# Kernel tuning notes

Hardware: AMD Instinct MI355X
Metric: run time of the kernel (lower is better)

Reference implementation:

```python
import jax, jax.numpy as jnp
import numpy as np

NUM_HEADS = 16
HEAD_DIM = 64  # hidden_size 1024 / 16 heads


def setup_inputs() -> dict:
    key = jax.random.key(0)
    ks = jax.random.split(key, 4)
    B, S, H = 2, 2048, 1024
    scale = 0.02
    return {
        "hidden_states": jax.random.normal(ks[0], (B, S, H), jnp.float32),
        "attention_mask": jnp.zeros((B, 1, 1, S), jnp.float32),  # additive mask
        "Wq": jax.random.normal(ks[1], (H, H), jnp.float32) * scale,
        "bq": jnp.zeros((H,), jnp.float32),
        "Wk": jax.random.normal(ks[2], (H, H), jnp.float32) * scale,
        "bk": jnp.zeros((H,), jnp.float32),
        "Wv": jax.random.normal(ks[3], (H, H), jnp.float32) * scale,
        "bv": jnp.zeros((H,), jnp.float32),
    }


def _split_heads(x):
    B, S, H = x.shape
    return x.reshape(B, S, NUM_HEADS, HEAD_DIM).transpose(0, 2, 1, 3)  # [B,h,S,dh]


def reference(hidden_states, attention_mask, Wq, bq, Wk, bk, Wv, bv):
    q = _split_heads(hidden_states @ Wq + bq)
    k = _split_heads(hidden_states @ Wk + bk)
    v = _split_heads(hidden_states @ Wv + bv)
    # scaled dot-product scores [B,h,S,S]
    scores = jnp.einsum("bhqd,bhkd->bhqk", q, k) / np.sqrt(HEAD_DIM).astype(np.float32)
    scores = scores + attention_mask  # additive mask, broadcast [B,1,1,S]
    probs = jax.nn.softmax(scores, axis=-1)  # dropout prob = 0.0
    ctx = jnp.einsum("bhqk,bhkd->bhqd", probs, v)
    B, h, S, dh = ctx.shape
    return ctx.transpose(0, 2, 1, 3).reshape(B, S, h * dh)  # [B,S,hidden]
```

## Files before the change

kernel.cpp:

```cpp
#include <hip/hip_runtime.h>
#include <hip/hip_bf16.h>


typedef __bf16 bf16x8 __attribute__((ext_vector_type(8)));
typedef __bf16 bf16x4 __attribute__((ext_vector_type(4)));
typedef float f32x4 __attribute__((ext_vector_type(4)));
typedef float f32x16 __attribute__((ext_vector_type(16)));
typedef int i32x4 __attribute__((ext_vector_type(4)));

static constexpr int H = 1024;
static constexpr int S = 2048;
static constexpr int NH = 16;
static constexpr int DH = 64;
static constexpr float L2E = 1.4426950408889634f;

#if __has_builtin(__builtin_amdgcn_exp2f)
#define EXP2F(x) __builtin_amdgcn_exp2f(x)
#else
#define EXP2F(x) __builtin_exp2f(x)
#endif

__device__ inline void gll16(const void* g, void* l) {
  __builtin_amdgcn_global_load_lds(
      (const __attribute__((address_space(1))) void*)g,
      (__attribute__((address_space(3))) void*)l, 16, 0, 0);
}

__device__ inline int pack2bf(float lo, float hi) {
  unsigned short a = __builtin_bit_cast(unsigned short, (__bf16)lo);
  unsigned short b = __builtin_bit_cast(unsigned short, (__bf16)hi);
  return (int)(((unsigned)b << 16) | (unsigned)a);
}

__device__ inline void plswap(int& a, int& b) {
  asm volatile("v_permlane32_swap_b32 %0, %1" : "+v"(a), "+v"(b));
}

__global__ __launch_bounds__(256) void convert_kernel(
    const float* __restrict__ X, const float* __restrict__ W0,
    const float* __restrict__ W1, const float* __restrict__ W2,
    __bf16* __restrict__ Xb, __bf16* __restrict__ Wt) {
  __shared__ float T[64][65];
  const int bid = blockIdx.x, tid = threadIdx.x;
  if (bid < 2048) {
    size_t i = ((size_t)bid * 256 + tid) * 8;
    float4 f0 = *(const float4*)(X + i);
    float4 f1 = *(const float4*)(X + i + 4);
    bf16x8 o;
    o[0] = (__bf16)f0.x; o[1] = (__bf16)f0.y; o[2] = (__bf16)f0.z; o[3] = (__bf16)f0.w;
    o[4] = (__bf16)f1.x; o[5] = (__bf16)f1.y; o[6] = (__bf16)f1.z; o[7] = (__bf16)f1.w;
    *(bf16x8*)(Xb + i) = o;
    return;
  }
  const int wid = bid - 2048;
  const int z = wid >> 8, t = wid & 255;
  const int k0 = (t >> 4) * 64, n0 = (t & 15) * 64;
  const float* W = z == 0 ? W0 : (z == 1 ? W1 : W2);
  __bf16* Wo = Wt + (size_t)z * H * H;
#pragma unroll
  for (int it = 0; it < 4; ++it) {
    int r = it * 16 + (tid >> 4), c = (tid & 15) * 4;
    *(float4*)&T[r][c] = *(const float4*)&W[(size_t)(k0 + r) * H + n0 + c];
  }
  __syncthreads();
#pragma unroll
  for (int it = 0; it < 4; ++it) {
    int n = it * 16 + (tid >> 4), c0 = (tid & 15) * 4;
    bf16x4 o;
#pragma unroll
    for (int j = 0; j < 4; ++j) o[j] = (__bf16)T[c0 + j][n];
    *(bf16x4*)&Wo[(size_t)(n0 + n) * H + k0 + c0] = o;
  }
}

__global__ __launch_bounds__(256, 3) void qkv_gemm_kernel(
    const __bf16* __restrict__ Xb, const __bf16* __restrict__ Wt,
    const float* __restrict__ bq, const float* __restrict__ bk,
    const float* __restrict__ bv,
    __bf16* __restrict__ Qt, __bf16* __restrict__ K, __bf16* __restrict__ Vt)
{
  __shared__ __bf16 As[128 * 64];
  __shared__ __bf16 Bs[128 * 64];

  const int tid = threadIdx.x, lane = tid & 63, w = tid >> 6;
  const int quad = lane >> 4, l16 = lane & 15;

  const int lin = blockIdx.x + 24 * blockIdx.y;
  const int swz = (lin & 7) * 96 + (lin >> 3);
  const int bx = swz >> 5;
  const int by = swz & 31;
  const int wsel = bx >> 3;
  const int n0 = (bx & 7) * 128;
  const int m0 = by * 128;
  const int wr = w & 1, wc = w >> 1;

  const __bf16* Wsel = Wt + (size_t)wsel * H * H;
  const float* bias = wsel == 0 ? bq : (wsel == 1 ? bk : bv);

  const __bf16* aptr[4];
  const __bf16* bptr[4];
#pragma unroll
  for (int i = 0; i < 4; ++i) {
    int s = w * 256 + i * 64 + lane;
    int row = s >> 3, col = s & 7, sc = col ^ (row & 7);
    aptr[i] = Xb + (size_t)(m0 + row) * H + sc * 8;
    bptr[i] = Wsel + (size_t)(n0 + row) * H + sc * 8;
  }

  f32x4 acc[4][4] = {};

  for (int k0 = 0; k0 < H; k0 += 64) {
    __syncthreads();
#pragma unroll
    for (int i = 0; i < 4; ++i) {
      gll16(aptr[i] + k0, &As[(w * 256 + i * 64) * 8]);
      gll16(bptr[i] + k0, &Bs[(w * 256 + i * 64) * 8]);
    }
    __syncthreads();
#pragma unroll
    for (int kc = 0; kc < 2; ++kc) {
      bf16x8 af[4], bfr[4];
#pragma unroll
      for (int t = 0; t < 4; ++t) {
        int ra = wr * 64 + t * 16 + l16;
        af[t] = *(const bf16x8*)&As[ra * 64 + (((kc * 4 + quad) ^ (ra & 7)) * 8)];
        int rb = wc * 64 + t * 16 + l16;
        bfr[t] = *(const bf16x8*)&Bs[rb * 64 + (((kc * 4 + quad) ^ (rb & 7)) * 8)];
      }
#pragma unroll
      for (int t = 0; t < 4; ++t)
#pragma unroll
        for (int u = 0; u < 4; ++u)
          acc[t][u] = __builtin_amdgcn_mfma_f32_16x16x32_bf16(af[t], bfr[u], acc[t][u], 0, 0, 0);
    }
  }

  const float qscale = 0.125f * L2E;
#pragma unroll
  for (int u = 0; u < 4; ++u) {
    int n = n0 + wc * 64 + u * 16 + l16;
    int head = n >> 6, d = n & 63;
    float bias_v = bias[n];
#pragma unroll
    for (int t = 0; t < 4; ++t) {
      int srow = m0 + wr * 64 + t * 16 + quad * 4;
      int b = srow >> 11, si = srow & (S - 1);
      int bh = b * NH + head;
      if (wsel == 1) {
        __bf16* dst = K + ((size_t)bh * S + si) * DH + d;
#pragma unroll
        for (int r = 0; r < 4; ++r)
          dst[(size_t)r * DH] = (__bf16)(acc[t][u][r] + bias_v);
      } else {
        float scl = wsel == 0 ? qscale : 1.0f;
        __bf16* outp = wsel == 0 ? Qt : Vt;
        bf16x4 o;
#pragma unroll
        for (int r = 0; r < 4; ++r) o[r] = (__bf16)((acc[t][u][r] + bias_v) * scl);
        *(bf16x4*)&outp[((size_t)bh * DH + d) * S + si] = o;
      }
    }
  }
}

__global__ __launch_bounds__(256, 4) void attn_kernel(
    const __bf16* __restrict__ Qt, const __bf16* __restrict__ K,
    const __bf16* __restrict__ Vt, const float* __restrict__ mask,
    float* __restrict__ out)
{
  __shared__ __bf16 SM[20480];
  __bf16* Ksb = SM;
  __bf16* Vsb = SM + 8192;
  float*  Ms  = (float*)(SM + 16384);

  const int tid = threadIdx.x, lane = tid & 63, w = tid >> 6;
  const int l31 = lane & 31, hi = lane >> 5;
  const int wl = w & 1, wh = w >> 1;

  const int lin = blockIdx.y * 32 + blockIdx.x;
  const int v = (lin & 7) * 128 + (lin >> 3);
  const int bh = v >> 5, b = bh >> 4, h = bh & 15;
  const int q0 = (v & 31) * 64;

  const __bf16* Qb = Qt + (size_t)bh * DH * S;
  const __bf16* Kb = K + (size_t)bh * S * DH;
  const __bf16* Vb = Vt + (size_t)bh * DH * S;
  const float* mb = mask + (size_t)b * S;

  {
    int idx = tid * 8;
    float4 m0v = *(const float4*)&mb[idx];
    float4 m1v = *(const float4*)&mb[idx + 4];
    float4 s0v = {m0v.x * L2E, m0v.y * L2E, m0v.z * L2E, m0v.w * L2E};
    float4 s1v = {m1v.x * L2E, m1v.y * L2E, m1v.z * L2E, m1v.w * L2E};
    *(float4*)&Ms[idx] = s0v;
    *(float4*)&Ms[idx + 4] = s1v;
  }

  const int q = q0 + wl * 32 + l31;
  bf16x8 qf[4];
#pragma unroll
  for (int kc = 0; kc < 4; ++kc)
#pragma unroll
    for (int j = 0; j < 8; ++j)
      qf[kc][j] = Qb[(size_t)(kc * 16 + hi * 8 + j) * S + q];

  const int kvbase = wh * 1024;
  const __bf16* kptr[4];
  const __bf16* vptr[4];
#pragma unroll
  for (int i = 0; i < 4; ++i) {
    int s = wl * 256 + i * 64 + lane;
    int row = s >> 3, col = s & 7, sc = col ^ (row & 7);
    kptr[i] = Kb + (size_t)(kvbase + row) * DH + sc * 8;
    vptr[i] = Vb + (size_t)row * S + kvbase + sc * 8;
  }

  f32x16 o0 = {}, o1 = {};
  float dl = 0.0f;

  for (int st = 0; st < 16; ++st) {
    __syncthreads();
#pragma unroll
    for (int i = 0; i < 4; ++i) {
      gll16(kptr[i] + (size_t)st * 64 * DH,
            &Ksb[wh * 4096 + (wl * 256 + i * 64 + lane) * 8]);
      gll16(vptr[i] + st * 64,
            &Vsb[wh * 4096 + (wl * 256 + i * 64 + lane) * 8]);
    }
    __syncthreads();
    const __bf16* Kc = &Ksb[wh * 4096];
    const __bf16* Vc = &Vsb[wh * 4096];
    const int kvabs = kvbase + st * 64;

#pragma unroll
    for (int kvsub = 0; kvsub < 2; ++kvsub) {
      const int rk = kvsub * 32 + l31;
      f32x16 cc;
#pragma unroll
      for (int g = 0; g < 4; ++g) {
        float4 m4 = *(const float4*)&Ms[kvabs + kvsub * 32 + g * 8 + hi * 4];
        cc[4 * g + 0] = m4.x; cc[4 * g + 1] = m4.y;
        cc[4 * g + 2] = m4.z; cc[4 * g + 3] = m4.w;
      }
      __builtin_amdgcn_s_setprio(1);
#pragma unroll
      for (int kc = 0; kc < 4; ++kc) {
        bf16x8 af = *(const bf16x8*)&Kc[rk * 64 + (((kc * 2 + hi) ^ (l31 & 7)) * 8)];
        cc = __builtin_amdgcn_mfma_f32_32x32x16_bf16(af, qf[kc], cc, 0, 0, 0);
      }
      __builtin_amdgcn_s_setprio(0);

      float p[16];
#pragma unroll
      for (int r = 0; r < 16; ++r) { p[r] = EXP2F(cc[r]); dl += p[r]; }
      int a0 = pack2bf(p[0],  p[1]),  b0 = pack2bf(p[2],  p[3]);
      int a1 = pack2bf(p[4],  p[5]),  b1 = pack2bf(p[6],  p[7]);
      int a2 = pack2bf(p[8],  p[9]),  b2 = pack2bf(p[10], p[11]);
      int a3 = pack2bf(p[12], p[13]), b3 = pack2bf(p[14], p[15]);
      plswap(a0, a1); plswap(b0, b1);
      plswap(a2, a3); plswap(b2, b3);
      i32x4 pi0 = {a0, b0, a1, b1};
      i32x4 pi1 = {a2, b2, a3, b3};
      bf16x8 pf0 = __builtin_bit_cast(bf16x8, pi0);
      bf16x8 pf1 = __builtin_bit_cast(bf16x8, pi1);

      __builtin_amdgcn_s_setprio(1);
#pragma unroll
      for (int pp = 0; pp < 2; ++pp) {
        const int pc = kvsub * 2 + pp;
        const bf16x8 pf = pp ? pf1 : pf0;
        bf16x8 vf0 = *(const bf16x8*)&Vc[l31 * 64 + (((pc * 2 + hi) ^ (l31 & 7)) * 8)];
        o0 = __builtin_amdgcn_mfma_f32_32x32x16_bf16(vf0, pf, o0, 0, 0, 0);
        bf16x8 vf1 = *(const bf16x8*)&Vc[(32 + l31) * 64 + (((pc * 2 + hi) ^ (l31 & 7)) * 8)];
        o1 = __builtin_amdgcn_mfma_f32_32x32x16_bf16(vf1, pf, o1, 0, 0, 0);
      }
      __builtin_amdgcn_s_setprio(0);
    }
  }

  float lsum = dl + __shfl_xor(dl, 32);

  __syncthreads();
  float* Os = (float*)SM;
  float* Ls = (float*)(SM + 16384);
  const int qi = wl * 32 + l31;
  if (wh == 1) {
#pragma unroll
    for (int g = 0; g < 4; ++g) {
      int s0 = (2 * g + hi) ^ (l31 & 7);
      float4 t0 = {o0[4 * g + 0], o0[4 * g + 1], o0[4 * g + 2], o0[4 * g + 3]};
      *(float4*)&Os[qi * 64 + s0 * 4] = t0;
      int s1 = (8 + 2 * g + hi) ^ (l31 & 7);
      float4 t1 = {o1[4 * g + 0], o1[4 * g + 1], o1[4 * g + 2], o1[4 * g + 3]};
      *(float4*)&Os[qi * 64 + s1 * 4] = t1;
    }
    if (hi == 0) Ls[qi] = lsum;
  }
  __syncthreads();
  if (wh == 0) {
    float ltot = lsum + Ls[qi];
    float invl = 1.0f / ltot;
#pragma unroll
    for (int g = 0; g < 4; ++g) {
      int d0 = g * 8 + hi * 4;
      int s0 = (2 * g + hi) ^ (l31 & 7);
      float4 u0 = *(const float4*)&Os[qi * 64 + s0 * 4];
      float4 r0 = {(o0[4 * g + 0] + u0.x) * invl, (o0[4 * g + 1] + u0.y) * invl,
                   (o0[4 * g + 2] + u0.z) * invl, (o0[4 * g + 3] + u0.w) * invl};
      *(float4*)&out[((size_t)b * S + q) * H + h * DH + d0] = r0;
      int s1 = (8 + 2 * g + hi) ^ (l31 & 7);
      float4 u1 = *(const float4*)&Os[qi * 64 + s1 * 4];
      float4 r1 = {(o1[4 * g + 0] + u1.x) * invl, (o1[4 * g + 1] + u1.y) * invl,
                   (o1[4 * g + 2] + u1.z) * invl, (o1[4 * g + 3] + u1.w) * invl};
      *(float4*)&out[((size_t)b * S + q) * H + h * DH + 32 + d0] = r1;
    }
  }
}

extern "C" void kernel_launch(void* const* d_in, const int* in_sizes, int n_in,
                              void* d_out, int out_size, void* d_ws, size_t ws_size,
                              hipStream_t stream) {
  const float* X    = (const float*)d_in[0];
  const float* mask = (const float*)d_in[1];
  const float* Wq   = (const float*)d_in[2];
  const float* bq   = (const float*)d_in[3];
  const float* Wk   = (const float*)d_in[4];
  const float* bk   = (const float*)d_in[5];
  const float* Wv   = (const float*)d_in[6];
  const float* bv   = (const float*)d_in[7];
  float* out = (float*)d_out;

  const size_t per = (size_t)2 * NH * S * DH;
  __bf16* Qws  = (__bf16*)d_ws;
  __bf16* Kws  = Qws + per;
  __bf16* Vtws = Kws + per;

  __bf16* Xb = (__bf16*)d_out;
  __bf16* Wt = Xb + per;

  convert_kernel<<<2816, 256, 0, stream>>>(X, Wq, Wk, Wv, Xb, Wt);
  qkv_gemm_kernel<<<dim3(24, 32), 256, 0, stream>>>(Xb, Wt, bq, bk, bv,
                                                    Qws, Kws, Vtws);
  attn_kernel<<<dim3(32, 32), 256, 0, stream>>>(Qws, Kws, Vtws, mask, out);
}
```

Before: 169.3 us.

## Give each wave private K/V LDS strips to drop block-wide barriers

Replaces the block-shared 64-key K/V tiles, which were loaded cooperatively and guarded by two __syncthreads per stage, with per-wave private 32-key strips that each wave loads into its own LDS region and waits on with s_waitcnt vmcnt(0). This removes the barrier cost from the inner loop. In exchange, the two waves sharing a KV half now each load the same K/V data, doubling global/L2 traffic. There is also no prefetch overlap, since every strip is loaded then immediately waited on. The V layout is re-swizzled for 32-wide rows.

```diff
diff --git a/kernel.cpp b/kernel.cpp
--- a/kernel.cpp
+++ b/kernel.cpp
@@ -169,13 +169,14 @@
     float* __restrict__ out)
 {
   __shared__ __bf16 SM[20480];
-  __bf16* Ksb = SM;
-  __bf16* Vsb = SM + 8192;
-  float*  Ms  = (float*)(SM + 16384);
+  float* Ms = (float*)(SM + 16384);
 
   const int tid = threadIdx.x, lane = tid & 63, w = tid >> 6;
   const int l31 = lane & 31, hi = lane >> 5;
   const int wl = w & 1, wh = w >> 1;
+
+  __bf16* KsW = SM + w * 2048;
+  __bf16* VsW = SM + 8192 + w * 2048;
 
   const int lin = blockIdx.y * 32 + blockIdx.x;
   const int v = (lin & 7) * 128 + (lin >> 3);
@@ -205,78 +206,77 @@
     for (int j = 0; j < 8; ++j)
       qf[kc][j] = Qb[(size_t)(kc * 16 + hi * 8 + j) * S + q];
 
+  __syncthreads();
+
   const int kvbase = wh * 1024;
   const __bf16* kptr[4];
   const __bf16* vptr[4];
 #pragma unroll
   for (int i = 0; i < 4; ++i) {
-    int s = wl * 256 + i * 64 + lane;
-    int row = s >> 3, col = s & 7, sc = col ^ (row & 7);
-    kptr[i] = Kb + (size_t)(kvbase + row) * DH + sc * 8;
-    vptr[i] = Vb + (size_t)row * S + kvbase + sc * 8;
+    int s = i * 64 + lane;
+    {
+      int row = s >> 3, col = s & 7, sc = col ^ (row & 7);
+      kptr[i] = Kb + (size_t)(kvbase + row) * DH + sc * 8;
+    }
+    {
+      int row = s >> 2, col = s & 3, sc = col ^ (row & 3);
+      vptr[i] = Vb + (size_t)row * S + kvbase + sc * 8;
+    }
   }
 
   f32x16 o0 = {}, o1 = {};
   float dl = 0.0f;
 
-  for (int st = 0; st < 16; ++st) {
-    __syncthreads();
+  for (int strip = 0; strip < 32; ++strip) {
 #pragma unroll
     for (int i = 0; i < 4; ++i) {
-      gll16(kptr[i] + (size_t)st * 64 * DH,
-            &Ksb[wh * 4096 + (wl * 256 + i * 64 + lane) * 8]);
-      gll16(vptr[i] + st * 64,
-            &Vsb[wh * 4096 + (wl * 256 + i * 64 + lane) * 8]);
-    }
-    __syncthreads();
-    const __bf16* Kc = &Ksb[wh * 4096];
-    const __bf16* Vc = &Vsb[wh * 4096];
-    const int kvabs = kvbase + st * 64;
-
-#pragma unroll
-    for (int kvsub = 0; kvsub < 2; ++kvsub) {
-      const int rk = kvsub * 32 + l31;
-      f32x16 cc;
-#pragma unroll
-      for (int g = 0; g < 4; ++g) {
-        float4 m4 = *(const float4*)&Ms[kvabs + kvsub * 32 + g * 8 + hi * 4];
-        cc[4 * g + 0] = m4.x; cc[4 * g + 1] = m4.y;
-        cc[4 * g + 2] = m4.z; cc[4 * g + 3] = m4.w;
-      }
-      __builtin_amdgcn_s_setprio(1);
-#pragma unroll
-      for (int kc = 0; kc < 4; ++kc) {
-        bf16x8 af = *(const bf16x8*)&Kc[rk * 64 + (((kc * 2 + hi) ^ (l31 & 7)) * 8)];
-        cc = __builtin_amdgcn_mfma_f32_32x32x16_bf16(af, qf[kc], cc, 0, 0, 0);
-      }
-      __builtin_amdgcn_s_setprio(0);
-
-      float p[16];
-#pragma unroll
-      for (int r = 0; r < 16; ++r) { p[r] = EXP2F(cc[r]); dl += p[r]; }
-      int a0 = pack2bf(p[0],  p[1]),  b0 = pack2bf(p[2],  p[3]);
-      int a1 = pack2bf(p[4],  p[5]),  b1 = pack2bf(p[6],  p[7]);
-      int a2 = pack2bf(p[8],  p[9]),  b2 = pack2bf(p[10], p[11]);
-      int a3 = pack2bf(p[12], p[13]), b3 = pack2bf(p[14], p[15]);
-      plswap(a0, a1); plswap(b0, b1);
-      plswap(a2, a3); plswap(b2, b3);
-      i32x4 pi0 = {a0, b0, a1, b1};
-      i32x4 pi1 = {a2, b2, a3, b3};
-      bf16x8 pf0 = __builtin_bit_cast(bf16x8, pi0);
-      bf16x8 pf1 = __builtin_bit_cast(bf16x8, pi1);
-
-      __builtin_amdgcn_s_setprio(1);
-#pragma unroll
-      for (int pp = 0; pp < 2; ++pp) {
-        const int pc = kvsub * 2 + pp;
-        const bf16x8 pf = pp ? pf1 : pf0;
-        bf16x8 vf0 = *(const bf16x8*)&Vc[l31 * 64 + (((pc * 2 + hi) ^ (l31 & 7)) * 8)];
-        o0 = __builtin_amdgcn_mfma_f32_32x32x16_bf16(vf0, pf, o0, 0, 0, 0);
-        bf16x8 vf1 = *(const bf16x8*)&Vc[(32 + l31) * 64 + (((pc * 2 + hi) ^ (l31 & 7)) * 8)];
-        o1 = __builtin_amdgcn_mfma_f32_32x32x16_bf16(vf1, pf, o1, 0, 0, 0);
-      }
-      __builtin_amdgcn_s_setprio(0);
-    }
+      gll16(kptr[i] + (size_t)strip * 32 * DH, &KsW[(i * 64 + lane) * 8]);
+      gll16(vptr[i] + strip * 32, &VsW[(i * 64 + lane) * 8]);
+    }
+    asm volatile("s_waitcnt vmcnt(0)" ::: "memory");
+    __builtin_amdgcn_sched_barrier(0);
+
+    const int kvabs = kvbase + strip * 32;
+
+    f32x16 cc;
+#pragma unroll
+    for (int g = 0; g < 4; ++g) {
+      float4 m4 = *(const float4*)&Ms[kvabs + g * 8 + hi * 4];
+      cc[4 * g + 0] = m4.x; cc[4 * g + 1] = m4.y;
+      cc[4 * g + 2] = m4.z; cc[4 * g + 3] = m4.w;
+    }
+    __builtin_amdgcn_s_setprio(1);
+#pragma unroll
+    for (int kc = 0; kc < 4; ++kc) {
+      bf16x8 af = *(const bf16x8*)&KsW[l31 * 64 + (((kc * 2 + hi) ^ (l31 & 7)) * 8)];
+      cc = __builtin_amdgcn_mfma_f32_32x32x16_bf16(af, qf[kc], cc, 0, 0, 0);
+    }
+    __builtin_amdgcn_s_setprio(0);
+
+    float p[16];
+#pragma unroll
+    for (int r = 0; r < 16; ++r) { p[r] = EXP2F(cc[r]); dl += p[r]; }
+    int a0 = pack2bf(p[0],  p[1]),  b0 = pack2bf(p[2],  p[3]);
+    int a1 = pack2bf(p[4],  p[5]),  b1 = pack2bf(p[6],  p[7]);
+    int a2 = pack2bf(p[8],  p[9]),  b2 = pack2bf(p[10], p[11]);
+    int a3 = pack2bf(p[12], p[13]), b3 = pack2bf(p[14], p[15]);
+    plswap(a0, a1); plswap(b0, b1);
+    plswap(a2, a3); plswap(b2, b3);
+    i32x4 pi0 = {a0, b0, a1, b1};
+    i32x4 pi1 = {a2, b2, a3, b3};
+    bf16x8 pf0 = __builtin_bit_cast(bf16x8, pi0);
+    bf16x8 pf1 = __builtin_bit_cast(bf16x8, pi1);
+
+    __builtin_amdgcn_s_setprio(1);
+#pragma unroll
+    for (int pp = 0; pp < 2; ++pp) {
+      const bf16x8 pf = pp ? pf1 : pf0;
+      bf16x8 vf0 = *(const bf16x8*)&VsW[l31 * 32 + (((pp * 2 + hi) ^ (l31 & 3)) * 8)];
+      o0 = __builtin_amdgcn_mfma_f32_32x32x16_bf16(vf0, pf, o0, 0, 0, 0);
+      bf16x8 vf1 = *(const bf16x8*)&VsW[(32 + l31) * 32 + (((pp * 2 + hi) ^ (l31 & 3)) * 8)];
+      o1 = __builtin_amdgcn_mfma_f32_32x32x16_bf16(vf1, pf, o1, 0, 0, 0);
+    }
+    __builtin_amdgcn_s_setprio(0);
   }
 
   float lsum = dl + __shfl_xor(dl, 32);
```

After: 183.5 us. 1.08x slower.
